# Optimization experiments

Hardware: AMD Instinct MI355X
Metric: run time of the kernel (lower is better)

## Reference

```python
import jax, jax.numpy as jnp
import numpy as np

G, N, E, F_IN, F_OUT, C = 256, 512, 4096, 64, 64, 16


def setup_inputs() -> dict:
    key = jax.random.key(0)
    ks = jax.random.split(key, 6)
    x_batch = jax.random.normal(ks[0], (G, N, F_IN), dtype=jnp.float32)
    edge_index_batch = jax.random.randint(ks[1], (G, 2, E), 0, N, dtype=jnp.int32)
    conv_weight = jax.random.normal(ks[2], (F_OUT, F_IN), dtype=jnp.float32) * (1.0 / np.sqrt(F_IN))
    conv_bias = jax.random.normal(ks[3], (F_OUT,), dtype=jnp.float32) * 0.02
    lin_weight = jax.random.normal(ks[4], (C, F_OUT * N), dtype=jnp.float32) * (1.0 / np.sqrt(F_OUT * N))
    lin_bias = jax.random.normal(ks[5], (C,), dtype=jnp.float32) * 0.02
    return {"x_batch": x_batch, "edge_index_batch": edge_index_batch,
            "conv_weight": conv_weight, "conv_bias": conv_bias,
            "lin_weight": lin_weight, "lin_bias": lin_bias}


def _gcn_conv_graph(xw, edge_index, self_loops):
    # xw: [N, F_OUT] (already linearly transformed), edge_index: [2, E]
    row = jnp.concatenate([edge_index[0], self_loops])  # sources
    col = jnp.concatenate([edge_index[1], self_loops])  # targets
    ones = jnp.ones(row.shape[0], dtype=xw.dtype)
    deg = jax.ops.segment_sum(ones, col, num_segments=N)  # degree at target nodes
    dinv = jnp.where(deg > 0, jax.lax.rsqrt(deg), jnp.zeros_like(deg))
    norm = dinv[row] * dinv[col]                          # [E+N]
    msgs = xw[row] * norm[:, None]                        # gather + normalize
    return jax.ops.segment_sum(msgs, col, num_segments=N)  # scatter-add at targets


def reference(x_batch, edge_index_batch, conv_weight, conv_bias, lin_weight, lin_bias):
    # GCNConv (PyG defaults: self-loops, symmetric normalization, post-agg bias)
    xw = jnp.einsum('gnf,of->gno', x_batch, conv_weight)  # [G, N, F_OUT]
    self_loops = jnp.arange(N, dtype=edge_index_batch.dtype)
    h = jax.vmap(_gcn_conv_graph, in_axes=(0, 0, None))(xw, edge_index_batch, self_loops)
    h = h + conv_bias
    h = jax.nn.relu(h)
    flat = h.reshape(h.shape[0], -1)                      # [G, N*F_OUT]
    logits = flat @ lin_weight.T + lin_bias               # [G, C]
    return jax.nn.log_softmax(logits, axis=-1)
```

## Files before the change

### kernel.cpp

```cpp
#include <hip/hip_runtime.h>

#define Gn 256
#define Nn 512
#define En 4096
#define Fn 64
#define Cn 16
#define ET (En + Nn)
#define EPAD 4616

typedef _Float16 halfv8 __attribute__((ext_vector_type(8)));
typedef _Float16 halfv4 __attribute__((ext_vector_type(4)));
typedef float    f32x4  __attribute__((ext_vector_type(4)));

__device__ __forceinline__ float pk_norm(unsigned p) {
    return (float)__builtin_bit_cast(_Float16, (unsigned short)(p & 0xffffu));
}

__global__ __launch_bounds__(256) void cvt_x(const float* __restrict__ x,
                                             _Float16* __restrict__ xc) {
    size_t base = (size_t)blockIdx.x * 256 + threadIdx.x;
    #pragma unroll
    for (int it = 0; it < 4; ++it) {
        size_t i = base + (size_t)it * (2048 * 256);
        float4 v = ((const float4*)x)[i];
        halfv4 h; h[0]=(_Float16)v.x; h[1]=(_Float16)v.y;
                  h[2]=(_Float16)v.z; h[3]=(_Float16)v.w;
        ((halfv4*)xc)[i] = h;
    }
}

__global__ __launch_bounds__(256) void cvt_lw_perm(const float* __restrict__ lw,
                                                   _Float16* __restrict__ lwh) {
    int u = blockIdx.x * 256 + threadIdx.x;
    int c = u >> 13, v = u & 8191;
    int jobidx = v >> 6, q = (v >> 4) & 3, m = v & 15;
    int n = (jobidx >> 2) * 16 + m;
    int o = (jobidx & 3) * 16 + q * 4;
    float4 f = *(const float4*)(lw + (size_t)c * (Nn * Fn) + n * 64 + o);
    halfv4 h; h[0]=(_Float16)f.x; h[1]=(_Float16)f.y;
              h[2]=(_Float16)f.z; h[3]=(_Float16)f.w;
    *(halfv4*)(lwh + (size_t)c * (Nn * Fn) + (size_t)v * 4) = h;
}

__global__ __launch_bounds__(256) void build_csr(const int* __restrict__ ei,
                                                 unsigned* __restrict__ epkG,
                                                 int* __restrict__ cntG) {
    __shared__ int      degL[Nn];
    __shared__ float    dinvL[Nn];
    __shared__ int      cntE[Nn];
    __shared__ unsigned epkL[ET];
    __shared__ int      wsum[4];
    const int g = blockIdx.x, tid = threadIdx.x;
    const int lane = tid & 63, wid = tid >> 6;
    const int* es = ei + (size_t)g * 2 * En;
    const int* ed = es + En;

    degL[tid] = 0; degL[tid + 256] = 0;
    __syncthreads();
    for (int e = tid; e < En; e += 256) atomicAdd(&degL[ed[e]], 1);
    __syncthreads();

    const int t2 = tid * 2;
    int cA = degL[t2] + 1, cB = degL[t2 + 1] + 1;
    dinvL[t2]     = rsqrtf((float)cA);
    dinvL[t2 + 1] = rsqrtf((float)cB);
    int p = cA + cB, v = p;
    #pragma unroll
    for (int off = 1; off < 64; off <<= 1) {
        int u = __shfl_up(v, off, 64);
        if (lane >= off) v += u;
    }
    if (lane == 63) wsum[wid] = v;
    __syncthreads();
    if (tid == 0) { int a = 0; for (int i = 0; i < 4; ++i) { int t = wsum[i]; wsum[i] = a; a += t; } }
    __syncthreads();
    int pe = v - p + wsum[wid];
    cntE[t2] = pe;
    cntE[t2 + 1] = pe + cA;
    __syncthreads();

    for (int e = tid; e < ET; e += 256) {
        int s, t;
        if (e < En) { s = es[e]; t = ed[e]; } else { s = t = e - En; }
        float nrm = dinvL[s] * dinvL[t];
        int slot = atomicAdd(&cntE[t], 1);
        unsigned short nb = __builtin_bit_cast(unsigned short, (_Float16)nrm);
        epkL[slot] = ((unsigned)s << 16) | nb;
    }
    __syncthreads();

    for (int i = tid; i < ET; i += 256) epkG[(size_t)g * EPAD + i] = epkL[i];
    cntG[(size_t)g * Nn + t2]     = cntE[t2];
    cntG[(size_t)g * Nn + t2 + 1] = cntE[t2 + 1];
}

__global__ __launch_bounds__(512, 4) void agg_conv(
    const _Float16* __restrict__ xc,
    const unsigned* __restrict__ epkG,
    const int*      __restrict__ cntG,
    const float*    __restrict__ w,
    const float*    __restrict__ wbias,
    _Float16* __restrict__ hout)
{
    __shared__ unsigned short xhs[256 * Fn];
    __shared__ unsigned short wts[Fn * Fn];
    __shared__ unsigned epkL[ET + 16];
    __shared__ int cntl[260];
    const int hh = blockIdx.x, g = blockIdx.y;
    const int tid = threadIdx.x, lane = tid & 63, wid = tid >> 6;
    const int tbase = hh * 256;

    const int slotlo = (hh == 0) ? 0 : cntG[(size_t)g * Nn + tbase - 1];
    const int slothi = cntG[(size_t)g * Nn + tbase + 255];
    const int total  = slothi - slotlo;

    if (tid < 257)
        cntl[tid] = (tid == 0) ? slotlo : cntG[(size_t)g * Nn + tbase + tid - 1];
    for (int i = tid; i < total; i += 512)
        epkL[i] = epkG[(size_t)g * EPAD + slotlo + i];
    {
        int o = tid >> 3, b8 = tid & 7;
        float4 va = *(const float4*)(w + o * Fn + b8 * 8);
        float4 vb = *(const float4*)(w + o * Fn + b8 * 8 + 4);
        halfv8 hv; hv[0]=(_Float16)va.x; hv[1]=(_Float16)va.y;
                   hv[2]=(_Float16)va.z; hv[3]=(_Float16)va.w;
                   hv[4]=(_Float16)vb.x; hv[5]=(_Float16)vb.y;
                   hv[6]=(_Float16)vb.z; hv[7]=(_Float16)vb.w;
        *(halfv8*)((char*)wts + o * 128 + ((b8 ^ (o & 7)) * 16)) = hv;
    }
    __syncthreads();

    {
        const _Float16* xgc = xc + (size_t)g * (Nn * Fn);
        const int qid = lane >> 4, fl = lane & 15;
        for (int r = 0; r < 8; ++r) {
            int tl = r * 32 + wid * 4 + qid;
            int beg = cntl[tl] - slotlo;
            int end = cntl[tl + 1] - slotlo;
            float a0 = 0.f, a1 = 0.f, a2 = 0.f, a3 = 0.f;
            unsigned pA0 = epkL[beg],     pA1 = epkL[beg + 1];
            unsigned pA2 = epkL[beg + 2], pA3 = epkL[beg + 3];
            int j = beg;
            for (; j + 4 <= end; j += 4) {
                unsigned pB0 = epkL[j + 4], pB1 = epkL[j + 5];
                unsigned pB2 = epkL[j + 6], pB3 = epkL[j + 7];
                int s0 = pA0 >> 16, s1 = pA1 >> 16, s2 = pA2 >> 16, s3 = pA3 >> 16;
                float n0 = pk_norm(pA0), n1 = pk_norm(pA1);
                float n2 = pk_norm(pA2), n3 = pk_norm(pA3);
                halfv4 x0 = *(const halfv4*)(xgc + s0 * Fn + fl * 4);
                halfv4 x1 = *(const halfv4*)(xgc + s1 * Fn + fl * 4);
                halfv4 x2 = *(const halfv4*)(xgc + s2 * Fn + fl * 4);
                halfv4 x3 = *(const halfv4*)(xgc + s3 * Fn + fl * 4);
                a0 += n0 * (float)x0[0] + n1 * (float)x1[0] + n2 * (float)x2[0] + n3 * (float)x3[0];
                a1 += n0 * (float)x0[1] + n1 * (float)x1[1] + n2 * (float)x2[1] + n3 * (float)x3[1];
                a2 += n0 * (float)x0[2] + n1 * (float)x1[2] + n2 * (float)x2[2] + n3 * (float)x3[2];
                a3 += n0 * (float)x0[3] + n1 * (float)x1[3] + n2 * (float)x2[3] + n3 * (float)x3[3];
                pA0 = pB0; pA1 = pB1; pA2 = pB2; pA3 = pB3;
            }
            for (; j < end; ++j) {
                int s = pA0 >> 16;
                float nm = pk_norm(pA0);
                halfv4 xv = *(const halfv4*)(xgc + s * Fn + fl * 4);
                a0 += nm * (float)xv[0]; a1 += nm * (float)xv[1];
                a2 += nm * (float)xv[2]; a3 += nm * (float)xv[3];
                pA0 = pA1; pA1 = pA2; pA2 = pA3;
            }
            halfv4 hv; hv[0]=(_Float16)a0; hv[1]=(_Float16)a1;
                       hv[2]=(_Float16)a2; hv[3]=(_Float16)a3;
            int dw = tl * 32 + (((fl >> 1) ^ (tl & 7)) * 4) + (fl & 1) * 2;
            *(halfv4*)((char*)xhs + dw * 4) = hv;
        }
    }
    __syncthreads();

    {
        const int m = lane & 15, q = lane >> 4;
        #pragma unroll
        for (int j = 0; j < 8; ++j) {
            int idx = wid * 8 + j;
            int tm = idx >> 2, to = idx & 3;
            int n = tm * 16 + m;
            int o = to * 16 + m;
            halfv8 X0 = *(const halfv8*)((const char*)xhs + n * 128 + ((q       ^ (n & 7)) * 16));
            halfv8 X1 = *(const halfv8*)((const char*)xhs + n * 128 + (((4 + q) ^ (n & 7)) * 16));
            halfv8 W0 = *(const halfv8*)((const char*)wts + o * 128 + ((q       ^ (o & 7)) * 16));
            halfv8 W1 = *(const halfv8*)((const char*)wts + o * 128 + (((4 + q) ^ (o & 7)) * 16));
            f32x4 acc = {0.f, 0.f, 0.f, 0.f};
            acc = __builtin_amdgcn_mfma_f32_16x16x32_f16(W0, X0, acc, 0, 0, 0);
            acc = __builtin_amdgcn_mfma_f32_16x16x32_f16(W1, X1, acc, 0, 0, 0);
            float4 bq = *(const float4*)&wbias[to * 16 + q * 4];
            halfv4 hv;
            hv[0] = (_Float16)fmaxf(acc[0] + bq.x, 0.0f);
            hv[1] = (_Float16)fmaxf(acc[1] + bq.y, 0.0f);
            hv[2] = (_Float16)fmaxf(acc[2] + bq.z, 0.0f);
            hv[3] = (_Float16)fmaxf(acc[3] + bq.w, 0.0f);
            size_t off = (size_t)g * (Nn * Fn)
                       + (size_t)(((hh * 16 + tm) * 4 + to) * 256 + lane * 4);
            *(halfv4*)(hout + off) = hv;
        }
    }
}

__global__ __launch_bounds__(256) void linear_mfma(
    const _Float16* __restrict__ h,
    const _Float16* __restrict__ lwh,
    float* __restrict__ part)
{
    __shared__ float red[4][64][4];
    const int cx = blockIdx.x, gy = blockIdx.y;
    const int tid = threadIdx.x, lane = tid & 63, wid = tid >> 6;
    const int ml = lane & 15, q = lane >> 4;
    const size_t kbase = (size_t)cx * 1024 + wid * 256;
    const _Float16* ha = h   + (size_t)(gy * 16 + ml) * (Nn * Fn) + kbase + q * 8;
    const _Float16* lb = lwh + (size_t)ml * (Nn * Fn) + kbase + q * 8;

    f32x4 acc = {0.f, 0.f, 0.f, 0.f};
    #pragma unroll
    for (int ks = 0; ks < 8; ++ks) {
        halfv8 a = *(const halfv8*)(ha + ks * 32);
        halfv8 b = *(const halfv8*)(lb + ks * 32);
        acc = __builtin_amdgcn_mfma_f32_16x16x32_f16(a, b, acc, 0, 0, 0);
    }
    #pragma unroll
    for (int r = 0; r < 4; ++r) red[wid][lane][r] = acc[r];
    __syncthreads();
    {
        int m = tid >> 4, cc = tid & 15;
        int sl = (m >> 2) * 16 + cc, rg = m & 3;
        float v = red[0][sl][rg] + red[1][sl][rg] + red[2][sl][rg] + red[3][sl][rg];
        part[((size_t)(gy * 16 + m) * 32 + cx) * Cn + cc] = v;
    }
}

__global__ __launch_bounds__(64) void gcn_softmax(
    const float* __restrict__ part, const float* __restrict__ lbias,
    float* __restrict__ out)
{
    const int g = blockIdx.x, lane = threadIdx.x;
    if (lane < Cn) {
        float v = lbias[lane];
        #pragma unroll
        for (int s = 0; s < 32; ++s) v += part[((size_t)g * 32 + s) * Cn + lane];
        float m = v;
        #pragma unroll
        for (int off = 8; off > 0; off >>= 1) m = fmaxf(m, __shfl_xor(m, off, 16));
        float ex = expf(v - m);
        float ssum = ex;
        #pragma unroll
        for (int off = 8; off > 0; off >>= 1) ssum += __shfl_xor(ssum, off, 16);
        out[g * Cn + lane] = v - m - logf(ssum);
    }
}

extern "C" void kernel_launch(void* const* d_in, const int* in_sizes, int n_in,
                              void* d_out, int out_size, void* d_ws, size_t ws_size,
                              hipStream_t stream) {
    const float* x  = (const float*)d_in[0];
    const int*   ei = (const int*)d_in[1];
    const float* w  = (const float*)d_in[2];
    const float* wb = (const float*)d_in[3];
    const float* lw = (const float*)d_in[4];
    const float* lb = (const float*)d_in[5];
    float* out = (float*)d_out;

    char* wsp = (char*)d_ws;
    _Float16* xc   = (_Float16*)(wsp);
    _Float16* lwh  = (_Float16*)(wsp + 16777216);
    unsigned* epkG = (unsigned*)(wsp + 17825792);
    int*      cntG = (int*)     (wsp + 22552576);
    _Float16* hbuf = (_Float16*)(wsp + 23076864);
    float*    part = (float*)   (wsp + 39854080);

    hipLaunchKernelGGL(cvt_x,       dim3(2048),    dim3(256), 0, stream, x, xc);
    hipLaunchKernelGGL(cvt_lw_perm, dim3(512),     dim3(256), 0, stream, lw, lwh);
    hipLaunchKernelGGL(build_csr,   dim3(Gn),      dim3(256), 0, stream, ei, epkG, cntG);
    hipLaunchKernelGGL(agg_conv,    dim3(2, Gn),   dim3(512), 0, stream,
                       xc, epkG, cntG, w, wb, hbuf);
    hipLaunchKernelGGL(linear_mfma, dim3(32, 16),  dim3(256), 0, stream,
                       hbuf, lwh, part);
    hipLaunchKernelGGL(gcn_softmax, dim3(Gn),      dim3(64),  0, stream,
                       part, lb, out);
}
```

Baseline: 134.4 us.

## Drop x fp16 pre-conversion, split aggregation and conv kernels, fold lw conversion

Removes the separate cvt_x pass and has the gather kernel read fp32 x directly, writing the aggregated features as fp16 to global memory. The MFMA conv moves into its own kernel. That kernel also performs the linear-weight fp16 permutation in an extra grid column, which eliminates the cvt_lw_perm launch. The intent is to avoid a full read-write pass over x. The trade-off is that the gather now reads twice the bytes per neighbor, and an intermediate buffer is round-tripped through global memory.

```diff
diff --git a/kernel.cpp b/kernel.cpp
--- a/kernel.cpp
+++ b/kernel.cpp
@@ -3,7 +3,6 @@
 #define Gn 256
 #define Nn 512
 #define En 4096
-#define Fn 64
 #define Cn 16
 #define ET (En + Nn)
 #define EPAD 4616
@@ -14,32 +13,6 @@
 
 __device__ __forceinline__ float pk_norm(unsigned p) {
     return (float)__builtin_bit_cast(_Float16, (unsigned short)(p & 0xffffu));
-}
-
-__global__ __launch_bounds__(256) void cvt_x(const float* __restrict__ x,
-                                             _Float16* __restrict__ xc) {
-    size_t base = (size_t)blockIdx.x * 256 + threadIdx.x;
-    #pragma unroll
-    for (int it = 0; it < 4; ++it) {
-        size_t i = base + (size_t)it * (2048 * 256);
-        float4 v = ((const float4*)x)[i];
-        halfv4 h; h[0]=(_Float16)v.x; h[1]=(_Float16)v.y;
-                  h[2]=(_Float16)v.z; h[3]=(_Float16)v.w;
-        ((halfv4*)xc)[i] = h;
-    }
-}
-
-__global__ __launch_bounds__(256) void cvt_lw_perm(const float* __restrict__ lw,
-                                                   _Float16* __restrict__ lwh) {
-    int u = blockIdx.x * 256 + threadIdx.x;
-    int c = u >> 13, v = u & 8191;
-    int jobidx = v >> 6, q = (v >> 4) & 3, m = v & 15;
-    int n = (jobidx >> 2) * 16 + m;
-    int o = (jobidx & 3) * 16 + q * 4;
-    float4 f = *(const float4*)(lw + (size_t)c * (Nn * Fn) + n * 64 + o);
-    halfv4 h; h[0]=(_Float16)f.x; h[1]=(_Float16)f.y;
-              h[2]=(_Float16)f.z; h[3]=(_Float16)f.w;
-    *(halfv4*)(lwh + (size_t)c * (Nn * Fn) + (size_t)v * 4) = h;
 }
 
 __global__ __launch_bounds__(256) void build_csr(const int* __restrict__ ei,
@@ -94,17 +67,13 @@
     cntG[(size_t)g * Nn + t2 + 1] = cntE[t2 + 1];
 }
 
-__global__ __launch_bounds__(512, 4) void agg_conv(
-    const _Float16* __restrict__ xc,
+__global__ __launch_bounds__(512) void gather_k(
+    const float*    __restrict__ x,
     const unsigned* __restrict__ epkG,
     const int*      __restrict__ cntG,
-    const float*    __restrict__ w,
-    const float*    __restrict__ wbias,
-    _Float16* __restrict__ hout)
-{
-    __shared__ unsigned short xhs[256 * Fn];
-    __shared__ unsigned short wts[Fn * Fn];
-    __shared__ unsigned epkL[ET + 16];
+    _Float16* __restrict__ xhg)
+{
+    __shared__ unsigned epkL[ET + 8];
     __shared__ int cntl[260];
     const int hh = blockIdx.x, g = blockIdx.y;
     const int tid = threadIdx.x, lane = tid & 63, wid = tid >> 6;
@@ -118,86 +87,124 @@
         cntl[tid] = (tid == 0) ? slotlo : cntG[(size_t)g * Nn + tbase + tid - 1];
     for (int i = tid; i < total; i += 512)
         epkL[i] = epkG[(size_t)g * EPAD + slotlo + i];
-    {
-        int o = tid >> 3, b8 = tid & 7;
-        float4 va = *(const float4*)(w + o * Fn + b8 * 8);
-        float4 vb = *(const float4*)(w + o * Fn + b8 * 8 + 4);
+    __syncthreads();
+
+    const float* xgf = x + (size_t)g * (Nn * 64);
+    const int qid = lane >> 4, fl = lane & 15;
+    for (int r = 0; r < 8; ++r) {
+        int tl = r * 32 + wid * 4 + qid;
+        int beg = cntl[tl] - slotlo;
+        int end = cntl[tl + 1] - slotlo;
+        float a0 = 0.f, a1 = 0.f, a2 = 0.f, a3 = 0.f;
+        unsigned pA0 = epkL[beg],     pA1 = epkL[beg + 1];
+        unsigned pA2 = epkL[beg + 2], pA3 = epkL[beg + 3];
+        int j = beg;
+        for (; j + 4 <= end; j += 4) {
+            unsigned pB0 = epkL[j + 4], pB1 = epkL[j + 5];
+            unsigned pB2 = epkL[j + 6], pB3 = epkL[j + 7];
+            int s0 = pA0 >> 16, s1 = pA1 >> 16, s2 = pA2 >> 16, s3 = pA3 >> 16;
+            float n0 = pk_norm(pA0), n1 = pk_norm(pA1);
+            float n2 = pk_norm(pA2), n3 = pk_norm(pA3);
+            float4 x0 = *(const float4*)(xgf + s0 * 64 + fl * 4);
+            float4 x1 = *(const float4*)(xgf + s1 * 64 + fl * 4);
+            float4 x2 = *(const float4*)(xgf + s2 * 64 + fl * 4);
+            float4 x3 = *(const float4*)(xgf + s3 * 64 + fl * 4);
+            a0 += n0 * x0.x + n1 * x1.x + n2 * x2.x + n3 * x3.x;
+            a1 += n0 * x0.y + n1 * x1.y + n2 * x2.y + n3 * x3.y;
+            a2 += n0 * x0.z + n1 * x1.z + n2 * x2.z + n3 * x3.z;
+            a3 += n0 * x0.w + n1 * x1.w + n2 * x2.w + n3 * x3.w;
+            pA0 = pB0; pA1 = pB1; pA2 = pB2; pA3 = pB3;
+        }
+        for (; j < end; ++j) {
+            int s = pA0 >> 16;
+            float nm = pk_norm(pA0);
+            float4 xv = *(const float4*)(xgf + s * 64 + fl * 4);
+            a0 += nm * xv.x; a1 += nm * xv.y; a2 += nm * xv.z; a3 += nm * xv.w;
+            pA0 = pA1; pA1 = pA2; pA2 = pA3;
+        }
+        halfv4 hv; hv[0]=(_Float16)a0; hv[1]=(_Float16)a1;
+                   hv[2]=(_Float16)a2; hv[3]=(_Float16)a3;
+        *(halfv4*)(xhg + (size_t)g * 32768 + (tbase + tl) * 64 + fl * 4) = hv;
+    }
+}
+
+__global__ __launch_bounds__(256) void conv_k(
+    const _Float16* __restrict__ xhg,
+    const float*    __restrict__ w,
+    const float*    __restrict__ wbias,
+    const float*    __restrict__ lw,
+    _Float16* __restrict__ lwh,
+    _Float16* __restrict__ hout)
+{
+    __shared__ unsigned short xhs[256 * 64];
+    __shared__ unsigned short wts[64 * 64];
+    const int hh = blockIdx.x, g = blockIdx.y;
+    const int tid = threadIdx.x, lane = tid & 63, wid = tid >> 6;
+
+    if (hh == 2) {
+        int u0 = (g * 256 + tid) * 2;
+        #pragma unroll
+        for (int r = 0; r < 2; ++r) {
+            int idx = u0 + r;
+            int c = idx >> 13, v4 = idx & 8191;
+            int jobidx = v4 >> 6, q = (v4 >> 4) & 3, m = v4 & 15;
+            int n = (jobidx >> 2) * 16 + m;
+            int o = (jobidx & 3) * 16 + q * 4;
+            float4 f = *(const float4*)(lw + (size_t)c * 32768 + n * 64 + o);
+            halfv4 h; h[0]=(_Float16)f.x; h[1]=(_Float16)f.y;
+                      h[2]=(_Float16)f.z; h[3]=(_Float16)f.w;
+            *(halfv4*)(lwh + (size_t)c * 32768 + (size_t)v4 * 4) = h;
+        }
+        return;
+    }
+
+    #pragma unroll
+    for (int it = 0; it < 2; ++it) {
+        int idx = tid + it * 256;
+        int o = idx >> 3, b8 = idx & 7;
+        float4 va = *(const float4*)(w + o * 64 + b8 * 8);
+        float4 vb = *(const float4*)(w + o * 64 + b8 * 8 + 4);
         halfv8 hv; hv[0]=(_Float16)va.x; hv[1]=(_Float16)va.y;
                    hv[2]=(_Float16)va.z; hv[3]=(_Float16)va.w;
                    hv[4]=(_Float16)vb.x; hv[5]=(_Float16)vb.y;
                    hv[6]=(_Float16)vb.z; hv[7]=(_Float16)vb.w;
         *(halfv8*)((char*)wts + o * 128 + ((b8 ^ (o & 7)) * 16)) = hv;
     }
-    __syncthreads();
-
     {
-        const _Float16* xgc = xc + (size_t)g * (Nn * Fn);
-        const int qid = lane >> 4, fl = lane & 15;
-        for (int r = 0; r < 8; ++r) {
-            int tl = r * 32 + wid * 4 + qid;
-            int beg = cntl[tl] - slotlo;
-            int end = cntl[tl + 1] - slotlo;
-            float a0 = 0.f, a1 = 0.f, a2 = 0.f, a3 = 0.f;
-            unsigned pA0 = epkL[beg],     pA1 = epkL[beg + 1];
-            unsigned pA2 = epkL[beg + 2], pA3 = epkL[beg + 3];
-            int j = beg;
-            for (; j + 4 <= end; j += 4) {
-                unsigned pB0 = epkL[j + 4], pB1 = epkL[j + 5];
-                unsigned pB2 = epkL[j + 6], pB3 = epkL[j + 7];
-                int s0 = pA0 >> 16, s1 = pA1 >> 16, s2 = pA2 >> 16, s3 = pA3 >> 16;
-                float n0 = pk_norm(pA0), n1 = pk_norm(pA1);
-                float n2 = pk_norm(pA2), n3 = pk_norm(pA3);
-                halfv4 x0 = *(const halfv4*)(xgc + s0 * Fn + fl * 4);
-                halfv4 x1 = *(const halfv4*)(xgc + s1 * Fn + fl * 4);
-                halfv4 x2 = *(const halfv4*)(xgc + s2 * Fn + fl * 4);
-                halfv4 x3 = *(const halfv4*)(xgc + s3 * Fn + fl * 4);
-                a0 += n0 * (float)x0[0] + n1 * (float)x1[0] + n2 * (float)x2[0] + n3 * (float)x3[0];
-                a1 += n0 * (float)x0[1] + n1 * (float)x1[1] + n2 * (float)x2[1] + n3 * (float)x3[1];
-                a2 += n0 * (float)x0[2] + n1 * (float)x1[2] + n2 * (float)x2[2] + n3 * (float)x3[2];
-                a3 += n0 * (float)x0[3] + n1 * (float)x1[3] + n2 * (float)x2[3] + n3 * (float)x3[3];
-                pA0 = pB0; pA1 = pB1; pA2 = pB2; pA3 = pB3;
-            }
-            for (; j < end; ++j) {
-                int s = pA0 >> 16;
-                float nm = pk_norm(pA0);
-                halfv4 xv = *(const halfv4*)(xgc + s * Fn + fl * 4);
-                a0 += nm * (float)xv[0]; a1 += nm * (float)xv[1];
-                a2 += nm * (float)xv[2]; a3 += nm * (float)xv[3];
-                pA0 = pA1; pA1 = pA2; pA2 = pA3;
-            }
-            halfv4 hv; hv[0]=(_Float16)a0; hv[1]=(_Float16)a1;
-                       hv[2]=(_Float16)a2; hv[3]=(_Float16)a3;
-            int dw = tl * 32 + (((fl >> 1) ^ (tl & 7)) * 4) + (fl & 1) * 2;
-            *(halfv4*)((char*)xhs + dw * 4) = hv;
-        }
-    }
-    __syncthreads();
-
-    {
-        const int m = lane & 15, q = lane >> 4;
-        #pragma unroll
-        for (int j = 0; j < 8; ++j) {
-            int idx = wid * 8 + j;
-            int tm = idx >> 2, to = idx & 3;
-            int n = tm * 16 + m;
-            int o = to * 16 + m;
-            halfv8 X0 = *(const halfv8*)((const char*)xhs + n * 128 + ((q       ^ (n & 7)) * 16));
-            halfv8 X1 = *(const halfv8*)((const char*)xhs + n * 128 + (((4 + q) ^ (n & 7)) * 16));
-            halfv8 W0 = *(const halfv8*)((const char*)wts + o * 128 + ((q       ^ (o & 7)) * 16));
-            halfv8 W1 = *(const halfv8*)((const char*)wts + o * 128 + (((4 + q) ^ (o & 7)) * 16));
-            f32x4 acc = {0.f, 0.f, 0.f, 0.f};
-            acc = __builtin_amdgcn_mfma_f32_16x16x32_f16(W0, X0, acc, 0, 0, 0);
-            acc = __builtin_amdgcn_mfma_f32_16x16x32_f16(W1, X1, acc, 0, 0, 0);
-            float4 bq = *(const float4*)&wbias[to * 16 + q * 4];
-            halfv4 hv;
-            hv[0] = (_Float16)fmaxf(acc[0] + bq.x, 0.0f);
-            hv[1] = (_Float16)fmaxf(acc[1] + bq.y, 0.0f);
-            hv[2] = (_Float16)fmaxf(acc[2] + bq.z, 0.0f);
-            hv[3] = (_Float16)fmaxf(acc[3] + bq.w, 0.0f);
-            size_t off = (size_t)g * (Nn * Fn)
-                       + (size_t)(((hh * 16 + tm) * 4 + to) * 256 + lane * 4);
-            *(halfv4*)(hout + off) = hv;
-        }
+        const _Float16* src = xhg + (size_t)g * 32768 + hh * 256 * 64;
+        #pragma unroll
+        for (int it = 0; it < 8; ++it) {
+            int u = tid + it * 256;
+            int b8 = u & 7, n = u >> 3;
+            halfv8 v = *(const halfv8*)(src + n * 64 + b8 * 8);
+            *(halfv8*)((char*)xhs + n * 128 + ((b8 ^ (n & 7)) * 16)) = v;
+        }
+    }
+    __syncthreads();
+
+    const int m = lane & 15, q = lane >> 4;
+    #pragma unroll
+    for (int j = 0; j < 16; ++j) {
+        int idx = wid * 16 + j;
+        int tm = idx >> 2, to = idx & 3;
+        int n = tm * 16 + m;
+        int o = to * 16 + m;
+        halfv8 X0 = *(const halfv8*)((const char*)xhs + n * 128 + ((q       ^ (n & 7)) * 16));
+        halfv8 X1 = *(const halfv8*)((const char*)xhs + n * 128 + (((4 + q) ^ (n & 7)) * 16));
+        halfv8 W0 = *(const halfv8*)((const char*)wts + o * 128 + ((q       ^ (o & 7)) * 16));
+        halfv8 W1 = *(const halfv8*)((const char*)wts + o * 128 + (((4 + q) ^ (o & 7)) * 16));
+        f32x4 acc = {0.f, 0.f, 0.f, 0.f};
+        acc = __builtin_amdgcn_mfma_f32_16x16x32_f16(W0, X0, acc, 0, 0, 0);
+        acc = __builtin_amdgcn_mfma_f32_16x16x32_f16(W1, X1, acc, 0, 0, 0);
+        float4 bq = *(const float4*)&wbias[to * 16 + q * 4];
+        halfv4 hv;
+        hv[0] = (_Float16)fmaxf(acc[0] + bq.x, 0.0f);
+        hv[1] = (_Float16)fmaxf(acc[1] + bq.y, 0.0f);
+        hv[2] = (_Float16)fmaxf(acc[2] + bq.z, 0.0f);
+        hv[3] = (_Float16)fmaxf(acc[3] + bq.w, 0.0f);
+        size_t off = (size_t)g * 32768
+                   + (size_t)((((hh * 16 + tm) * 4 + to) * 256) + lane * 4);
+        *(halfv4*)(hout + off) = hv;
     }
 }
 
@@ -211,8 +218,8 @@
     const int tid = threadIdx.x, lane = tid & 63, wid = tid >> 6;
     const int ml = lane & 15, q = lane >> 4;
     const size_t kbase = (size_t)cx * 1024 + wid * 256;
-    const _Float16* ha = h   + (size_t)(gy * 16 + ml) * (Nn * Fn) + kbase + q * 8;
-    const _Float16* lb = lwh + (size_t)ml * (Nn * Fn) + kbase + q * 8;
+    const _Float16* ha = h   + (size_t)(gy * 16 + ml) * 32768 + kbase + q * 8;
+    const _Float16* lb = lwh + (size_t)ml * 32768 + kbase + q * 8;
 
     f32x4 acc = {0.f, 0.f, 0.f, 0.f};
     #pragma unroll
@@ -264,20 +271,17 @@
     float* out = (float*)d_out;
 
     char* wsp = (char*)d_ws;
-    _Float16* xc   = (_Float16*)(wsp);
-    _Float16* lwh  = (_Float16*)(wsp + 16777216);
-    unsigned* epkG = (unsigned*)(wsp + 17825792);
-    int*      cntG = (int*)     (wsp + 22552576);
+    unsigned* epkG = (unsigned*)(wsp);
+    int*      cntG = (int*)     (wsp + 4726784);
+    _Float16* xhg  = (_Float16*)(wsp + 5251072);
+    _Float16* lwh  = (_Float16*)(wsp + 22028288);
     _Float16* hbuf = (_Float16*)(wsp + 23076864);
     float*    part = (float*)   (wsp + 39854080);
 
-    hipLaunchKernelGGL(cvt_x,       dim3(2048),    dim3(256), 0, stream, x, xc);
-    hipLaunchKernelGGL(cvt_lw_perm, dim3(512),     dim3(256), 0, stream, lw, lwh);
     hipLaunchKernelGGL(build_csr,   dim3(Gn),      dim3(256), 0, stream, ei, epkG, cntG);
-    hipLaunchKernelGGL(agg_conv,    dim3(2, Gn),   dim3(512), 0, stream,
-                       xc, epkG, cntG, w, wb, hbuf);
-    hipLaunchKernelGGL(linear_mfma, dim3(32, 16),  dim3(256), 0, stream,
-                       hbuf, lwh, part);
-    hipLaunchKernelGGL(gcn_softmax, dim3(Gn),      dim3(64),  0, stream,
-                       part, lb, out);
-}
+    hipLaunchKernelGGL(gather_k,    dim3(2, Gn),   dim3(512), 0, stream, x, epkG, cntG, xhg);
+    hipLaunchKernelGGL(conv_k,      dim3(3, Gn),   dim3(256), 0, stream,
+                       xhg, w, wb, lw, lwh, hbuf);
+    hipLaunchKernelGGL(linear_mfma, dim3(32, 16),  dim3(256), 0, stream, hbuf, lwh, part);
+    hipLaunchKernelGGL(gcn_softmax, dim3(Gn),      dim3(64),  0, stream, part, lb, out);
+}
```

New measurement: 138.0 us. 1.03x slower.
